# Optimization experiments

Hardware: AMD Instinct MI355X
Metric: run time of the kernel (lower is better)

## Reference

```python
import jax, jax.numpy as jnp
import numpy as np

LN_EPS = 1e-5
LEAKY_SLOPE = 0.2


def setup_inputs() -> dict:
    key = jax.random.key(0)
    k = jax.random.split(key, 6)
    B, N, D, H, hd = 32768, 4, 256, 4, 64
    out_dim = H * hd
    # Weights stored as (in_dim, out_dim) so projection is h @ W (same math as torch Linear with W.T)
    return {
        "h": jax.random.normal(k[0], (B, N, D), dtype=jnp.float32),
        "edge_bias": jax.random.normal(k[1], (N, N), dtype=jnp.float32),
        "W_l": jax.random.normal(k[2], (D, out_dim), dtype=jnp.float32) * (1.0 / np.sqrt(D)),
        "W_r": jax.random.normal(k[3], (D, out_dim), dtype=jnp.float32) * (1.0 / np.sqrt(D)),
        "a": jax.random.normal(k[4], (H, hd), dtype=jnp.float32) * (1.0 / np.sqrt(hd)),
        "ln_gamma": jnp.ones((out_dim,), dtype=jnp.float32),
        "ln_beta": jnp.zeros((out_dim,), dtype=jnp.float32),
    }


def reference(h, edge_bias, W_l, W_r, a, ln_gamma, ln_beta):
    B, N, _ = h.shape
    H, d = a.shape
    g_l = (h @ W_l).reshape(B, N, H, d)
    g_r = (h @ W_r).reshape(B, N, H, d)
    # GATv2 dynamic attention: LeakyReLU applied BEFORE scoring with a
    pairwise = jax.nn.leaky_relu(g_l[:, :, None] + g_r[:, None, :], LEAKY_SLOPE)  # (B,N,N,H,d)
    e = jnp.einsum('bijhd,hd->bijh', pairwise, a)  # (B,N,N,H)
    e = e + edge_bias[None, :, :, None]
    alpha = jax.nn.softmax(e, axis=2)  # softmax over neighbor j
    # dropout is identity in eval mode
    h_prime = jnp.einsum('bijh,bjhd->bihd', alpha, g_r).reshape(B, N, H * d)
    # LayerNorm over last dim
    mu = jnp.mean(h_prime, axis=-1, keepdims=True)
    var = jnp.var(h_prime, axis=-1, keepdims=True)
    out = (h_prime - mu) * jax.lax.rsqrt(var + LN_EPS) * ln_gamma + ln_beta
    return out
```

## Files before the change

kernel.cpp:

```cpp
#include <hip/hip_runtime.h>
#include <hip/hip_bf16.h>

typedef short bf16x8 __attribute__((ext_vector_type(8)));
typedef float f32x4 __attribute__((ext_vector_type(4)));

#define LN_EPS 1e-5f
#define SLOPE 0.2f

__device__ __forceinline__ unsigned short f2bf(float f){
  __hip_bfloat16 b = __float2bfloat16(f);
  return *reinterpret_cast<unsigned short*>(&b);
}

__global__ void wconv_kernel(const float* __restrict__ Wl,
                             const float* __restrict__ Wr,
                             unsigned short* __restrict__ wbf){
  int idx = blockIdx.x * 256 + threadIdx.x;
  int c = idx & 511;
  int gg = (idx >> 9) & 3;
  int s = idx >> 11;
  int k0 = s * 32 + gg * 8;
  const float* src = (c < 256) ? (Wl + c) : (Wr + (c - 256));
  bf16x8 v;
  #pragma unroll
  for (int j = 0; j < 8; ++j) v[j] = (short)f2bf(src[(k0 + j) * 256]);
  *(bf16x8*)&wbf[(size_t)idx * 8] = v;
}

template<bool USE_WS>
__global__ __launch_bounds__(256, 2)
void gat_fused(const float* __restrict__ hin, const float* __restrict__ ebias,
               const float* __restrict__ Wl, const float* __restrict__ Wr,
               const float* __restrict__ avec, const float* __restrict__ gmw,
               const float* __restrict__ btw, const unsigned short* __restrict__ wbf,
               float* __restrict__ out){
  __shared__ __align__(16) unsigned short uni[8192];
  __shared__ float red1[128], red2[128];
  __shared__ float eb_s[16];

  const int t = threadIdx.x;
  const int lane = t & 63;
  const int w = t >> 6;
  const int b0 = blockIdx.x * 8;
  const int g = lane >> 4;
  const int ln = lane & 15;

  float av[4];
  #pragma unroll
  for (int c = 0; c < 4; ++c) av[c] = avec[w * 64 + c * 16 + ln];
  if (t < 16) eb_s[t] = ebias[t];

  {
    const float* hb = hin + (size_t)b0 * 1024;
    #pragma unroll
    for (int it = 0; it < 4; ++it){
      int q = it * 256 + t;
      int row = q >> 5;
      int c = q & 31;
      const float* src = hb + row * 256 + c * 8;
      float4 f0 = *(const float4*)src;
      float4 f1 = *(const float4*)(src + 4);
      bf16x8 v;
      v[0]=(short)f2bf(f0.x); v[1]=(short)f2bf(f0.y); v[2]=(short)f2bf(f0.z); v[3]=(short)f2bf(f0.w);
      v[4]=(short)f2bf(f1.x); v[5]=(short)f2bf(f1.y); v[6]=(short)f2bf(f1.z); v[7]=(short)f2bf(f1.w);
      *(bf16x8*)&uni[row * 256 + ((c ^ (row & 7)) << 3)] = v;
    }
  }
  __syncthreads();

  f32x4 acc[2][8];
  #pragma unroll
  for (int m = 0; m < 2; ++m)
    #pragma unroll
    for (int c = 0; c < 8; ++c)
      acc[m][c] = (f32x4){0.f, 0.f, 0.f, 0.f};

  if constexpr (USE_WS){
    const unsigned short* wbase = wbf + (size_t)g * 4096 + (size_t)(w * 64 + ln) * 8;
    bf16x8 af[2], afn[2], P[4], Q[4];
    #pragma unroll
    for (int m = 0; m < 2; ++m)
      af[m] = *(const bf16x8*)&uni[(m * 16 + ln) * 256 + ((g ^ (ln & 7)) << 3)];
    #pragma unroll
    for (int c = 0; c < 4; ++c)
      P[c] = *(const bf16x8*)(wbase + c * 128);

    #pragma unroll
    for (int step = 0; step < 8; ++step){
      const unsigned short* wp = wbase + (size_t)step * 16384;
      #pragma unroll
      for (int c = 0; c < 4; ++c)
        Q[c] = *(const bf16x8*)(wp + 2048 + c * 128);
      if (step < 7){
        #pragma unroll
        for (int m = 0; m < 2; ++m)
          afn[m] = *(const bf16x8*)&uni[(m * 16 + ln) * 256
                     + ((((step + 1) * 4 + g) ^ (ln & 7)) << 3)];
      }
      __builtin_amdgcn_s_setprio(1);
      #pragma unroll
      for (int m = 0; m < 2; ++m)
        #pragma unroll
        for (int c = 0; c < 4; ++c)
          acc[m][c] = __builtin_amdgcn_mfma_f32_16x16x32_bf16(af[m], P[c], acc[m][c], 0, 0, 0);
      __builtin_amdgcn_s_setprio(0);
      if (step < 7){
        const unsigned short* wpn = wp + 16384;
        #pragma unroll
        for (int c = 0; c < 4; ++c)
          P[c] = *(const bf16x8*)(wpn + c * 128);
      }
      __builtin_amdgcn_s_setprio(1);
      #pragma unroll
      for (int m = 0; m < 2; ++m)
        #pragma unroll
        for (int c = 0; c < 4; ++c)
          acc[m][c + 4] = __builtin_amdgcn_mfma_f32_16x16x32_bf16(af[m], Q[c], acc[m][c + 4], 0, 0, 0);
      __builtin_amdgcn_s_setprio(0);
      af[0] = afn[0]; af[1] = afn[1];
    }
  } else {
    for (int step = 0; step < 8; ++step){
      bf16x8 af[2], bfr[8];
      #pragma unroll
      for (int m = 0; m < 2; ++m){
        int row = m * 16 + ln;
        int chunk = step * 4 + g;
        af[m] = *(const bf16x8*)&uni[row * 256 + ((chunk ^ (row & 7)) << 3)];
      }
      #pragma unroll
      for (int c = 0; c < 4; ++c){
        int col = w * 64 + c * 16 + ln;
        #pragma unroll
        for (int j = 0; j < 8; ++j){
          bfr[c][j]     = (short)f2bf(Wl[(step * 32 + g * 8 + j) * 256 + col]);
          bfr[c + 4][j] = (short)f2bf(Wr[(step * 32 + g * 8 + j) * 256 + col]);
        }
      }
      #pragma unroll
      for (int m = 0; m < 2; ++m)
        #pragma unroll
        for (int c = 0; c < 8; ++c)
          acc[m][c] = __builtin_amdgcn_mfma_f32_16x16x32_bf16(af[m], bfr[c], acc[m][c], 0, 0, 0);
    }
  }

  #pragma unroll
  for (int m = 0; m < 2; ++m){
    float e[16];
    #pragma unroll
    for (int q = 0; q < 16; ++q) e[q] = 0.f;
    #pragma unroll
    for (int c = 0; c < 4; ++c){
      f32x4 GL = acc[m][c];
      f32x4 GR = acc[m][c + 4];
      #pragma unroll
      for (int i = 0; i < 4; ++i)
        #pragma unroll
        for (int j = 0; j < 4; ++j){
          float x = GL[i] + GR[j];
          x = fmaxf(x, SLOPE * x);
          e[i * 4 + j] = fmaf(x, av[c], e[i * 4 + j]);
        }
    }
    #pragma unroll
    for (int mask = 1; mask <= 8; mask <<= 1)
      #pragma unroll
      for (int q = 0; q < 16; ++q)
        e[q] += __shfl_xor(e[q], mask);
    #pragma unroll
    for (int q = 0; q < 16; ++q) e[q] += eb_s[q];
    #pragma unroll
    for (int i = 0; i < 4; ++i){
      float mx = fmaxf(fmaxf(e[i*4+0], e[i*4+1]), fmaxf(e[i*4+2], e[i*4+3]));
      float p0 = __expf(e[i*4+0] - mx);
      float p1 = __expf(e[i*4+1] - mx);
      float p2 = __expf(e[i*4+2] - mx);
      float p3 = __expf(e[i*4+3] - mx);
      float rs = 1.f / (p0 + p1 + p2 + p3);
      e[i*4+0] = p0 * rs; e[i*4+1] = p1 * rs; e[i*4+2] = p2 * rs; e[i*4+3] = p3 * rs;
    }
    float hp[4][4];
    #pragma unroll
    for (int i = 0; i < 4; ++i){
      #pragma unroll
      for (int c = 0; c < 4; ++c){
        f32x4 GR = acc[m][c + 4];
        float v = e[i*4+0] * GR[0];
        v = fmaf(e[i*4+1], GR[1], v);
        v = fmaf(e[i*4+2], GR[2], v);
        v = fmaf(e[i*4+3], GR[3], v);
        hp[i][c] = v;
      }
      float s1 = hp[i][0] + hp[i][1] + hp[i][2] + hp[i][3];
      float s2 = fmaf(hp[i][0], hp[i][0],
                 fmaf(hp[i][1], hp[i][1],
                 fmaf(hp[i][2], hp[i][2], hp[i][3] * hp[i][3])));
      #pragma unroll
      for (int mask = 1; mask <= 8; mask <<= 1){
        s1 += __shfl_xor(s1, mask);
        s2 += __shfl_xor(s2, mask);
      }
      int r = (m * 4 + g) * 4 + i;
      if (ln == 0){ red1[r * 4 + w] = s1; red2[r * 4 + w] = s2; }
    }
    __syncthreads();

    float gmr[4], btr[4];
    #pragma unroll
    for (int c = 0; c < 4; ++c){
      gmr[c] = gmw[w * 64 + c * 16 + ln];
      btr[c] = btw[w * 64 + c * 16 + ln];
    }
    #pragma unroll
    for (int i = 0; i < 4; ++i){
      int r = (m * 4 + g) * 4 + i;
      float4 v1 = *(const float4*)&red1[r * 4];
      float4 v2 = *(const float4*)&red2[r * 4];
      float s1 = (v1.x + v1.y) + (v1.z + v1.w);
      float s2 = (v2.x + v2.y) + (v2.z + v2.w);
      float mu = s1 * (1.f / 256.f);
      float var = s2 * (1.f / 256.f) - mu * mu;
      float inv = rsqrtf(var + LN_EPS);
      float* op = out + ((size_t)b0 * 4 + r) * 256 + w * 64 + ln;
      #pragma unroll
      for (int c = 0; c < 4; ++c)
        op[c * 16] = fmaf((hp[i][c] - mu) * inv, gmr[c], btr[c]);
    }
  }
}

extern "C" void kernel_launch(void* const* d_in, const int* in_sizes, int n_in,
                              void* d_out, int out_size, void* d_ws, size_t ws_size,
                              hipStream_t stream){
  const float* h  = (const float*)d_in[0];
  const float* eb = (const float*)d_in[1];
  const float* Wl = (const float*)d_in[2];
  const float* Wr = (const float*)d_in[3];
  const float* a  = (const float*)d_in[4];
  const float* gm = (const float*)d_in[5];
  const float* bt = (const float*)d_in[6];
  float* out = (float*)d_out;
  (void)n_in; (void)out_size;

  int B = in_sizes[0] / 1024;
  int nblk = B / 8;

  if (ws_size >= 262144){
    unsigned short* wbf = (unsigned short*)d_ws;
    wconv_kernel<<<64, 256, 0, stream>>>(Wl, Wr, wbf);
    gat_fused<true><<<nblk, 256, 0, stream>>>(h, eb, Wl, Wr, a, gm, bt, wbf, out);
  } else {
    gat_fused<false><<<nblk, 256, 0, stream>>>(h, eb, Wl, Wr, a, gm, bt, nullptr, out);
  }
}
```

Baseline: 95.62 us.

## Make GAT kernel persistent with double-buffered LDS prefetch of next tile

Turns the fused GAT kernel into a persistent grid-stride kernel capped at 768 blocks. Each block processes tiles in a loop and prefetches the next tile's h rows into a second LDS buffer while the softmax/LayerNorm epilogue of the current tile runs, so global load latency overlaps with compute. The LDS allocation doubles (32 KB for h), which may limit occupancy. The extra in-flight float4 registers may also raise register pressure under the 2-blocks-per-SM launch bound.

```diff
diff --git a/kernel.cpp b/kernel.cpp
--- a/kernel.cpp
+++ b/kernel.cpp
@@ -33,25 +33,28 @@
                const float* __restrict__ Wl, const float* __restrict__ Wr,
                const float* __restrict__ avec, const float* __restrict__ gmw,
                const float* __restrict__ btw, const unsigned short* __restrict__ wbf,
-               float* __restrict__ out){
-  __shared__ __align__(16) unsigned short uni[8192];
+               float* __restrict__ out, int ntiles){
+  __shared__ __align__(16) unsigned short uni[16384];
   __shared__ float red1[128], red2[128];
   __shared__ float eb_s[16];
 
   const int t = threadIdx.x;
   const int lane = t & 63;
   const int w = t >> 6;
-  const int b0 = blockIdx.x * 8;
   const int g = lane >> 4;
   const int ln = lane & 15;
+  const int stride = gridDim.x;
 
   float av[4];
   #pragma unroll
   for (int c = 0; c < 4; ++c) av[c] = avec[w * 64 + c * 16 + ln];
   if (t < 16) eb_s[t] = ebias[t];
 
+  int tile = blockIdx.x;
+  if (tile >= ntiles) return;
+
   {
-    const float* hb = hin + (size_t)b0 * 1024;
+    const float* hb = hin + (size_t)tile * 8192;
     #pragma unroll
     for (int it = 0; it < 4; ++it){
       int q = it * 256 + t;
@@ -66,167 +69,313 @@
       *(bf16x8*)&uni[row * 256 + ((c ^ (row & 7)) << 3)] = v;
     }
   }
-  __syncthreads();
-
-  f32x4 acc[2][8];
-  #pragma unroll
-  for (int m = 0; m < 2; ++m)
-    #pragma unroll
-    for (int c = 0; c < 8; ++c)
-      acc[m][c] = (f32x4){0.f, 0.f, 0.f, 0.f};
-
-  if constexpr (USE_WS){
-    const unsigned short* wbase = wbf + (size_t)g * 4096 + (size_t)(w * 64 + ln) * 8;
-    bf16x8 af[2], afn[2], P[4], Q[4];
+  int cur = 0;
+
+  for (;;){
+    __syncthreads();
+    unsigned short* ub = &uni[cur * 8192];
+
+    f32x4 acc[2][8];
     #pragma unroll
     for (int m = 0; m < 2; ++m)
-      af[m] = *(const bf16x8*)&uni[(m * 16 + ln) * 256 + ((g ^ (ln & 7)) << 3)];
-    #pragma unroll
-    for (int c = 0; c < 4; ++c)
-      P[c] = *(const bf16x8*)(wbase + c * 128);
-
-    #pragma unroll
-    for (int step = 0; step < 8; ++step){
-      const unsigned short* wp = wbase + (size_t)step * 16384;
+      #pragma unroll
+      for (int c = 0; c < 8; ++c)
+        acc[m][c] = (f32x4){0.f, 0.f, 0.f, 0.f};
+
+    if constexpr (USE_WS){
+      const unsigned short* wbase = wbf + (size_t)g * 4096 + (size_t)(w * 64 + ln) * 8;
+      bf16x8 af[2], afn[2], P[4], Q[4];
+      #pragma unroll
+      for (int m = 0; m < 2; ++m)
+        af[m] = *(const bf16x8*)&ub[(m * 16 + ln) * 256 + ((g ^ (ln & 7)) << 3)];
       #pragma unroll
       for (int c = 0; c < 4; ++c)
-        Q[c] = *(const bf16x8*)(wp + 2048 + c * 128);
-      if (step < 7){
+        P[c] = *(const bf16x8*)(wbase + c * 128);
+      #pragma unroll
+      for (int step = 0; step < 8; ++step){
+        const unsigned short* wp = wbase + (size_t)step * 16384;
+        #pragma unroll
+        for (int c = 0; c < 4; ++c)
+          Q[c] = *(const bf16x8*)(wp + 2048 + c * 128);
+        if (step < 7){
+          #pragma unroll
+          for (int m = 0; m < 2; ++m)
+            afn[m] = *(const bf16x8*)&ub[(m * 16 + ln) * 256
+                       + ((((step + 1) * 4 + g) ^ (ln & 7)) << 3)];
+        }
+        __builtin_amdgcn_s_setprio(1);
         #pragma unroll
         for (int m = 0; m < 2; ++m)
-          afn[m] = *(const bf16x8*)&uni[(m * 16 + ln) * 256
-                     + ((((step + 1) * 4 + g) ^ (ln & 7)) << 3)];
-      }
-      __builtin_amdgcn_s_setprio(1);
-      #pragma unroll
-      for (int m = 0; m < 2; ++m)
+          #pragma unroll
+          for (int c = 0; c < 4; ++c)
+            acc[m][c] = __builtin_amdgcn_mfma_f32_16x16x32_bf16(af[m], P[c], acc[m][c], 0, 0, 0);
+        __builtin_amdgcn_s_setprio(0);
+        if (step < 7){
+          const unsigned short* wpn = wp + 16384;
+          #pragma unroll
+          for (int c = 0; c < 4; ++c)
+            P[c] = *(const bf16x8*)(wpn + c * 128);
+        }
+        __builtin_amdgcn_s_setprio(1);
+        #pragma unroll
+        for (int m = 0; m < 2; ++m)
+          #pragma unroll
+          for (int c = 0; c < 4; ++c)
+            acc[m][c + 4] = __builtin_amdgcn_mfma_f32_16x16x32_bf16(af[m], Q[c], acc[m][c + 4], 0, 0, 0);
+        __builtin_amdgcn_s_setprio(0);
+        af[0] = afn[0]; af[1] = afn[1];
+      }
+    } else {
+      for (int step = 0; step < 8; ++step){
+        bf16x8 af[2], bfr[8];
+        #pragma unroll
+        for (int m = 0; m < 2; ++m){
+          int row = m * 16 + ln;
+          int chunk = step * 4 + g;
+          af[m] = *(const bf16x8*)&ub[row * 256 + ((chunk ^ (row & 7)) << 3)];
+        }
+        #pragma unroll
+        for (int c = 0; c < 4; ++c){
+          int col = w * 64 + c * 16 + ln;
+          #pragma unroll
+          for (int j = 0; j < 8; ++j){
+            bfr[c][j]     = (short)f2bf(Wl[(step * 32 + g * 8 + j) * 256 + col]);
+            bfr[c + 4][j] = (short)f2bf(Wr[(step * 32 + g * 8 + j) * 256 + col]);
+          }
+        }
+        #pragma unroll
+        for (int m = 0; m < 2; ++m)
+          #pragma unroll
+          for (int c = 0; c < 8; ++c)
+            acc[m][c] = __builtin_amdgcn_mfma_f32_16x16x32_bf16(af[m], bfr[c], acc[m][c], 0, 0, 0);
+      }
+    }
+
+    const int ntile = tile + stride;
+    const bool have = ntile < ntiles;
+    const float* nb = hin + (size_t)ntile * 8192;
+    unsigned short* un = &uni[(cur ^ 1) * 8192];
+    float4 hA0, hA1, hB0, hB1, hC0, hC1, hD0, hD1;
+    if (have){
+      int q0 = t;
+      int q1 = t + 256;
+      hA0 = *(const float4*)(nb + (q0 >> 5) * 256 + (q0 & 31) * 8);
+      hA1 = *(const float4*)(nb + (q0 >> 5) * 256 + (q0 & 31) * 8 + 4);
+      hB0 = *(const float4*)(nb + (q1 >> 5) * 256 + (q1 & 31) * 8);
+      hB1 = *(const float4*)(nb + (q1 >> 5) * 256 + (q1 & 31) * 8 + 4);
+    }
+
+    {
+      const int m = 0;
+      float e[16];
+      #pragma unroll
+      for (int q = 0; q < 16; ++q) e[q] = 0.f;
+      #pragma unroll
+      for (int c = 0; c < 4; ++c){
+        f32x4 GL = acc[m][c];
+        f32x4 GR = acc[m][c + 4];
+        #pragma unroll
+        for (int i = 0; i < 4; ++i)
+          #pragma unroll
+          for (int j = 0; j < 4; ++j){
+            float x = GL[i] + GR[j];
+            x = fmaxf(x, SLOPE * x);
+            e[i * 4 + j] = fmaf(x, av[c], e[i * 4 + j]);
+          }
+      }
+      #pragma unroll
+      for (int mask = 1; mask <= 8; mask <<= 1)
+        #pragma unroll
+        for (int q = 0; q < 16; ++q)
+          e[q] += __shfl_xor(e[q], mask);
+      #pragma unroll
+      for (int q = 0; q < 16; ++q) e[q] += eb_s[q];
+      #pragma unroll
+      for (int i = 0; i < 4; ++i){
+        float mx = fmaxf(fmaxf(e[i*4+0], e[i*4+1]), fmaxf(e[i*4+2], e[i*4+3]));
+        float p0 = __expf(e[i*4+0] - mx);
+        float p1 = __expf(e[i*4+1] - mx);
+        float p2 = __expf(e[i*4+2] - mx);
+        float p3 = __expf(e[i*4+3] - mx);
+        float rs = 1.f / (p0 + p1 + p2 + p3);
+        e[i*4+0] = p0 * rs; e[i*4+1] = p1 * rs; e[i*4+2] = p2 * rs; e[i*4+3] = p3 * rs;
+      }
+      float hp[4][4];
+      #pragma unroll
+      for (int i = 0; i < 4; ++i){
+        #pragma unroll
+        for (int c = 0; c < 4; ++c){
+          f32x4 GR = acc[m][c + 4];
+          float v = e[i*4+0] * GR[0];
+          v = fmaf(e[i*4+1], GR[1], v);
+          v = fmaf(e[i*4+2], GR[2], v);
+          v = fmaf(e[i*4+3], GR[3], v);
+          hp[i][c] = v;
+        }
+        float s1 = hp[i][0] + hp[i][1] + hp[i][2] + hp[i][3];
+        float s2 = fmaf(hp[i][0], hp[i][0],
+                   fmaf(hp[i][1], hp[i][1],
+                   fmaf(hp[i][2], hp[i][2], hp[i][3] * hp[i][3])));
+        #pragma unroll
+        for (int mask = 1; mask <= 8; mask <<= 1){
+          s1 += __shfl_xor(s1, mask);
+          s2 += __shfl_xor(s2, mask);
+        }
+        int r = (m * 4 + g) * 4 + i;
+        if (ln == 0){ red1[r * 4 + w] = s1; red2[r * 4 + w] = s2; }
+      }
+      __syncthreads();
+
+      if (have){
+        int q2 = t + 512;
+        int q3 = t + 768;
+        hC0 = *(const float4*)(nb + (q2 >> 5) * 256 + (q2 & 31) * 8);
+        hC1 = *(const float4*)(nb + (q2 >> 5) * 256 + (q2 & 31) * 8 + 4);
+        hD0 = *(const float4*)(nb + (q3 >> 5) * 256 + (q3 & 31) * 8);
+        hD1 = *(const float4*)(nb + (q3 >> 5) * 256 + (q3 & 31) * 8 + 4);
+        {
+          int q0 = t, row = q0 >> 5, c = q0 & 31;
+          bf16x8 v;
+          v[0]=(short)f2bf(hA0.x); v[1]=(short)f2bf(hA0.y); v[2]=(short)f2bf(hA0.z); v[3]=(short)f2bf(hA0.w);
+          v[4]=(short)f2bf(hA1.x); v[5]=(short)f2bf(hA1.y); v[6]=(short)f2bf(hA1.z); v[7]=(short)f2bf(hA1.w);
+          *(bf16x8*)&un[row * 256 + ((c ^ (row & 7)) << 3)] = v;
+        }
+        {
+          int q1 = t + 256, row = q1 >> 5, c = q1 & 31;
+          bf16x8 v;
+          v[0]=(short)f2bf(hB0.x); v[1]=(short)f2bf(hB0.y); v[2]=(short)f2bf(hB0.z); v[3]=(short)f2bf(hB0.w);
+          v[4]=(short)f2bf(hB1.x); v[5]=(short)f2bf(hB1.y); v[6]=(short)f2bf(hB1.z); v[7]=(short)f2bf(hB1.w);
+          *(bf16x8*)&un[row * 256 + ((c ^ (row & 7)) << 3)] = v;
+        }
+      }
+
+      float gmr[4], btr[4];
+      #pragma unroll
+      for (int c = 0; c < 4; ++c){
+        gmr[c] = gmw[w * 64 + c * 16 + ln];
+        btr[c] = btw[w * 64 + c * 16 + ln];
+      }
+      #pragma unroll
+      for (int i = 0; i < 4; ++i){
+        int r = (m * 4 + g) * 4 + i;
+        float4 v1 = *(const float4*)&red1[r * 4];
+        float4 v2 = *(const float4*)&red2[r * 4];
+        float s1 = (v1.x + v1.y) + (v1.z + v1.w);
+        float s2 = (v2.x + v2.y) + (v2.z + v2.w);
+        float mu = s1 * (1.f / 256.f);
+        float var = s2 * (1.f / 256.f) - mu * mu;
+        float inv = rsqrtf(var + LN_EPS);
+        float* op = out + ((size_t)tile * 32 + r) * 256 + w * 64 + ln;
         #pragma unroll
         for (int c = 0; c < 4; ++c)
-          acc[m][c] = __builtin_amdgcn_mfma_f32_16x16x32_bf16(af[m], P[c], acc[m][c], 0, 0, 0);
-      __builtin_amdgcn_s_setprio(0);
-      if (step < 7){
-        const unsigned short* wpn = wp + 16384;
+          op[c * 16] = fmaf((hp[i][c] - mu) * inv, gmr[c], btr[c]);
+      }
+    }
+
+    {
+      const int m = 1;
+      float e[16];
+      #pragma unroll
+      for (int q = 0; q < 16; ++q) e[q] = 0.f;
+      #pragma unroll
+      for (int c = 0; c < 4; ++c){
+        f32x4 GL = acc[m][c];
+        f32x4 GR = acc[m][c + 4];
+        #pragma unroll
+        for (int i = 0; i < 4; ++i)
+          #pragma unroll
+          for (int j = 0; j < 4; ++j){
+            float x = GL[i] + GR[j];
+            x = fmaxf(x, SLOPE * x);
+            e[i * 4 + j] = fmaf(x, av[c], e[i * 4 + j]);
+          }
+      }
+      #pragma unroll
+      for (int mask = 1; mask <= 8; mask <<= 1)
+        #pragma unroll
+        for (int q = 0; q < 16; ++q)
+          e[q] += __shfl_xor(e[q], mask);
+      #pragma unroll
+      for (int q = 0; q < 16; ++q) e[q] += eb_s[q];
+      #pragma unroll
+      for (int i = 0; i < 4; ++i){
+        float mx = fmaxf(fmaxf(e[i*4+0], e[i*4+1]), fmaxf(e[i*4+2], e[i*4+3]));
+        float p0 = __expf(e[i*4+0] - mx);
+        float p1 = __expf(e[i*4+1] - mx);
+        float p2 = __expf(e[i*4+2] - mx);
+        float p3 = __expf(e[i*4+3] - mx);
+        float rs = 1.f / (p0 + p1 + p2 + p3);
+        e[i*4+0] = p0 * rs; e[i*4+1] = p1 * rs; e[i*4+2] = p2 * rs; e[i*4+3] = p3 * rs;
+      }
+      float hp[4][4];
+      #pragma unroll
+      for (int i = 0; i < 4; ++i){
+        #pragma unroll
+        for (int c = 0; c < 4; ++c){
+          f32x4 GR = acc[m][c + 4];
+          float v = e[i*4+0] * GR[0];
+          v = fmaf(e[i*4+1], GR[1], v);
+          v = fmaf(e[i*4+2], GR[2], v);
+          v = fmaf(e[i*4+3], GR[3], v);
+          hp[i][c] = v;
+        }
+        float s1 = hp[i][0] + hp[i][1] + hp[i][2] + hp[i][3];
+        float s2 = fmaf(hp[i][0], hp[i][0],
+                   fmaf(hp[i][1], hp[i][1],
+                   fmaf(hp[i][2], hp[i][2], hp[i][3] * hp[i][3])));
+        #pragma unroll
+        for (int mask = 1; mask <= 8; mask <<= 1){
+          s1 += __shfl_xor(s1, mask);
+          s2 += __shfl_xor(s2, mask);
+        }
+        int r = (m * 4 + g) * 4 + i;
+        if (ln == 0){ red1[r * 4 + w] = s1; red2[r * 4 + w] = s2; }
+      }
+      __syncthreads();
+
+      if (have){
+        {
+          int q2 = t + 512, row = q2 >> 5, c = q2 & 31;
+          bf16x8 v;
+          v[0]=(short)f2bf(hC0.x); v[1]=(short)f2bf(hC0.y); v[2]=(short)f2bf(hC0.z); v[3]=(short)f2bf(hC0.w);
+          v[4]=(short)f2bf(hC1.x); v[5]=(short)f2bf(hC1.y); v[6]=(short)f2bf(hC1.z); v[7]=(short)f2bf(hC1.w);
+          *(bf16x8*)&un[row * 256 + ((c ^ (row & 7)) << 3)] = v;
+        }
+        {
+          int q3 = t + 768, row = q3 >> 5, c = q3 & 31;
+          bf16x8 v;
+          v[0]=(short)f2bf(hD0.x); v[1]=(short)f2bf(hD0.y); v[2]=(short)f2bf(hD0.z); v[3]=(short)f2bf(hD0.w);
+          v[4]=(short)f2bf(hD1.x); v[5]=(short)f2bf(hD1.y); v[6]=(short)f2bf(hD1.z); v[7]=(short)f2bf(hD1.w);
+          *(bf16x8*)&un[row * 256 + ((c ^ (row & 7)) << 3)] = v;
+        }
+      }
+
+      float gmr[4], btr[4];
+      #pragma unroll
+      for (int c = 0; c < 4; ++c){
+        gmr[c] = gmw[w * 64 + c * 16 + ln];
+        btr[c] = btw[w * 64 + c * 16 + ln];
+      }
+      #pragma unroll
+      for (int i = 0; i < 4; ++i){
+        int r = (m * 4 + g) * 4 + i;
+        float4 v1 = *(const float4*)&red1[r * 4];
+        float4 v2 = *(const float4*)&red2[r * 4];
+        float s1 = (v1.x + v1.y) + (v1.z + v1.w);
+        float s2 = (v2.x + v2.y) + (v2.z + v2.w);
+        float mu = s1 * (1.f / 256.f);
+        float var = s2 * (1.f / 256.f) - mu * mu;
+        float inv = rsqrtf(var + LN_EPS);
+        float* op = out + ((size_t)tile * 32 + r) * 256 + w * 64 + ln;
         #pragma unroll
         for (int c = 0; c < 4; ++c)
-          P[c] = *(const bf16x8*)(wpn + c * 128);
-      }
-      __builtin_amdgcn_s_setprio(1);
-      #pragma unroll
-      for (int m = 0; m < 2; ++m)
-        #pragma unroll
-        for (int c = 0; c < 4; ++c)
-          acc[m][c + 4] = __builtin_amdgcn_mfma_f32_16x16x32_bf16(af[m], Q[c], acc[m][c + 4], 0, 0, 0);
-      __builtin_amdgcn_s_setprio(0);
-      af[0] = afn[0]; af[1] = afn[1];
+          op[c * 16] = fmaf((hp[i][c] - mu) * inv, gmr[c], btr[c]);
+      }
     }
-  } else {
-    for (int step = 0; step < 8; ++step){
-      bf16x8 af[2], bfr[8];
-      #pragma unroll
-      for (int m = 0; m < 2; ++m){
-        int row = m * 16 + ln;
-        int chunk = step * 4 + g;
-        af[m] = *(const bf16x8*)&uni[row * 256 + ((chunk ^ (row & 7)) << 3)];
-      }
-      #pragma unroll
-      for (int c = 0; c < 4; ++c){
-        int col = w * 64 + c * 16 + ln;
-        #pragma unroll
-        for (int j = 0; j < 8; ++j){
-          bfr[c][j]     = (short)f2bf(Wl[(step * 32 + g * 8 + j) * 256 + col]);
-          bfr[c + 4][j] = (short)f2bf(Wr[(step * 32 + g * 8 + j) * 256 + col]);
-        }
-      }
-      #pragma unroll
-      for (int m = 0; m < 2; ++m)
-        #pragma unroll
-        for (int c = 0; c < 8; ++c)
-          acc[m][c] = __builtin_amdgcn_mfma_f32_16x16x32_bf16(af[m], bfr[c], acc[m][c], 0, 0, 0);
-    }
-  }
-
-  #pragma unroll
-  for (int m = 0; m < 2; ++m){
-    float e[16];
-    #pragma unroll
-    for (int q = 0; q < 16; ++q) e[q] = 0.f;
-    #pragma unroll
-    for (int c = 0; c < 4; ++c){
-      f32x4 GL = acc[m][c];
-      f32x4 GR = acc[m][c + 4];
-      #pragma unroll
-      for (int i = 0; i < 4; ++i)
-        #pragma unroll
-        for (int j = 0; j < 4; ++j){
-          float x = GL[i] + GR[j];
-          x = fmaxf(x, SLOPE * x);
-          e[i * 4 + j] = fmaf(x, av[c], e[i * 4 + j]);
-        }
-    }
-    #pragma unroll
-    for (int mask = 1; mask <= 8; mask <<= 1)
-      #pragma unroll
-      for (int q = 0; q < 16; ++q)
-        e[q] += __shfl_xor(e[q], mask);
-    #pragma unroll
-    for (int q = 0; q < 16; ++q) e[q] += eb_s[q];
-    #pragma unroll
-    for (int i = 0; i < 4; ++i){
-      float mx = fmaxf(fmaxf(e[i*4+0], e[i*4+1]), fmaxf(e[i*4+2], e[i*4+3]));
-      float p0 = __expf(e[i*4+0] - mx);
-      float p1 = __expf(e[i*4+1] - mx);
-      float p2 = __expf(e[i*4+2] - mx);
-      float p3 = __expf(e[i*4+3] - mx);
-      float rs = 1.f / (p0 + p1 + p2 + p3);
-      e[i*4+0] = p0 * rs; e[i*4+1] = p1 * rs; e[i*4+2] = p2 * rs; e[i*4+3] = p3 * rs;
-    }
-    float hp[4][4];
-    #pragma unroll
-    for (int i = 0; i < 4; ++i){
-      #pragma unroll
-      for (int c = 0; c < 4; ++c){
-        f32x4 GR = acc[m][c + 4];
-        float v = e[i*4+0] * GR[0];
-        v = fmaf(e[i*4+1], GR[1], v);
-        v = fmaf(e[i*4+2], GR[2], v);
-        v = fmaf(e[i*4+3], GR[3], v);
-        hp[i][c] = v;
-      }
-      float s1 = hp[i][0] + hp[i][1] + hp[i][2] + hp[i][3];
-      float s2 = fmaf(hp[i][0], hp[i][0],
-                 fmaf(hp[i][1], hp[i][1],
-                 fmaf(hp[i][2], hp[i][2], hp[i][3] * hp[i][3])));
-      #pragma unroll
-      for (int mask = 1; mask <= 8; mask <<= 1){
-        s1 += __shfl_xor(s1, mask);
-        s2 += __shfl_xor(s2, mask);
-      }
-      int r = (m * 4 + g) * 4 + i;
-      if (ln == 0){ red1[r * 4 + w] = s1; red2[r * 4 + w] = s2; }
-    }
-    __syncthreads();
-
-    float gmr[4], btr[4];
-    #pragma unroll
-    for (int c = 0; c < 4; ++c){
-      gmr[c] = gmw[w * 64 + c * 16 + ln];
-      btr[c] = btw[w * 64 + c * 16 + ln];
-    }
-    #pragma unroll
-    for (int i = 0; i < 4; ++i){
-      int r = (m * 4 + g) * 4 + i;
-      float4 v1 = *(const float4*)&red1[r * 4];
-      float4 v2 = *(const float4*)&red2[r * 4];
-      float s1 = (v1.x + v1.y) + (v1.z + v1.w);
-      float s2 = (v2.x + v2.y) + (v2.z + v2.w);
-      float mu = s1 * (1.f / 256.f);
-      float var = s2 * (1.f / 256.f) - mu * mu;
-      float inv = rsqrtf(var + LN_EPS);
-      float* op = out + ((size_t)b0 * 4 + r) * 256 + w * 64 + ln;
-      #pragma unroll
-      for (int c = 0; c < 4; ++c)
-        op[c * 16] = fmaf((hp[i][c] - mu) * inv, gmr[c], btr[c]);
-    }
+
+    if (!have) break;
+    tile = ntile;
+    cur ^= 1;
   }
 }
 
@@ -244,13 +393,14 @@
   (void)n_in; (void)out_size;
 
   int B = in_sizes[0] / 1024;
-  int nblk = B / 8;
+  int ntiles = B / 8;
 
   if (ws_size >= 262144){
     unsigned short* wbf = (unsigned short*)d_ws;
     wconv_kernel<<<64, 256, 0, stream>>>(Wl, Wr, wbf);
-    gat_fused<true><<<nblk, 256, 0, stream>>>(h, eb, Wl, Wr, a, gm, bt, wbf, out);
+    int nblk = (ntiles < 768) ? ntiles : 768;
+    gat_fused<true><<<nblk, 256, 0, stream>>>(h, eb, Wl, Wr, a, gm, bt, wbf, out, ntiles);
   } else {
-    gat_fused<false><<<nblk, 256, 0, stream>>>(h, eb, Wl, Wr, a, gm, bt, nullptr, out);
+    gat_fused<false><<<ntiles, 256, 0, stream>>>(h, eb, Wl, Wr, a, gm, bt, nullptr, out, ntiles);
   }
 }
```

Result: slower. 297.9 us (+211.6%).
